# Performance work log

Hardware: AMD Instinct MI355X
Metric: run time of the kernel (lower is better)

## Reference

```python
import jax, jax.numpy as jnp
import numpy as np

INPUT_DIM = 2048
CLASSES = 1000
BATCH = 8192


def setup_inputs() -> dict:
    key = jax.random.key(0)
    kx, ky, kwx, kbx, kwy, kby = jax.random.split(key, 6)
    s_in = 1.0 / np.sqrt(INPUT_DIM)
    return {
        "x": jax.random.normal(kx, (BATCH, INPUT_DIM), dtype=jnp.float32),
        "y": jax.random.normal(ky, (BATCH, INPUT_DIM), dtype=jnp.float32),
        "Wx": jax.random.uniform(kwx, (CLASSES, INPUT_DIM), jnp.float32, -s_in, s_in),
        "bx": jax.random.uniform(kbx, (CLASSES,), jnp.float32, -s_in, s_in),
        "Wy": jax.random.uniform(kwy, (CLASSES, INPUT_DIM), jnp.float32, -s_in, s_in),
        "by": jax.random.uniform(kby, (CLASSES,), jnp.float32, -s_in, s_in),
    }


def _ds_combin_two(alpha1, alpha2, classes):
    # alpha1, alpha2: [B, C] Dirichlet params
    S1 = jnp.sum(alpha1, axis=1, keepdims=True)  # [B,1]
    S2 = jnp.sum(alpha2, axis=1, keepdims=True)
    b1 = (alpha1 - 1.0) / S1                      # belief masses [B,C]
    b2 = (alpha2 - 1.0) / S2
    u1 = classes / S1                             # uncertainty [B,1]
    u2 = classes / S2
    # bb_sum = sum_{i,j} b1_i b2_j = (sum b1)(sum b2); bb_diag = sum_i b1_i b2_i
    bb_sum = jnp.sum(b1, axis=1) * jnp.sum(b2, axis=1)   # [B]
    bb_diag = jnp.sum(b1 * b2, axis=1)                    # [B]
    C = (bb_sum - bb_diag)[:, None]                       # conflict [B,1]
    denom = 1.0 - C
    b_a = (b1 * b2 + b1 * u2 + b2 * u1) / denom           # [B,C]
    u_a = (u1 * u2) / denom                               # [B,1]
    S_a = classes / u_a                                   # [B,1]
    return b_a * S_a + 1.0                                # alpha_a [B,C]


def reference(x, y, Wx, bx, Wy, by):
    out_x = x @ Wx.T + bx                 # [B,C]
    out_y = y @ Wy.T + by
    alpha_x = jax.nn.softplus(out_x) + 1.0
    alpha_y = jax.nn.softplus(out_y) + 1.0
    alpha_a = _ds_combin_two(alpha_x, alpha_y, CLASSES)
    return (alpha_a, alpha_x, alpha_y)
```

## Files before the change

kernel.cpp:

```cpp
#include <hip/hip_runtime.h>
#include <hip/hip_bf16.h>
#include <math.h>

#define BATCH_N 8192
#define K_DIM   2048
#define CLS     1000

typedef __attribute__((ext_vector_type(8))) short short8;
typedef __attribute__((ext_vector_type(8))) unsigned short ushort8;
typedef __attribute__((ext_vector_type(4))) float floatx4;

static __device__ __forceinline__ float softplus_fast(float z) {
    return fmaxf(z, 0.f) + __logf(1.f + __expf(-fabsf(z)));
}


constexpr int NT = K_DIM / 32;

#define BARX  __builtin_amdgcn_s_barrier()
#define LGKM0 asm volatile("s_waitcnt lgkmcnt(0)" ::: "memory")
#define SB0   __builtin_amdgcn_sched_barrier(0)
#define PRIO1 __builtin_amdgcn_s_setprio(1)
#define PRIO0 __builtin_amdgcn_s_setprio(0)

__global__ __launch_bounds__(256, 2)
void gemm_fused(const float* __restrict__ Xa, const float* __restrict__ Xb,
                const float* __restrict__ Wa, const float* __restrict__ Wb,
                const float* __restrict__ biasa, const float* __restrict__ biasb,
                float* __restrict__ outa, float* __restrict__ outb)
{
    int flat = blockIdx.x + 8 * (blockIdx.y + 64 * blockIdx.z);
    int sw   = (flat & 7) * 128 + (flat >> 3);
    const int bx = sw & 7, by = (sw >> 3) & 63, bz = sw >> 9;

    const float* A    = bz ? Xb : Xa;
    const float* B    = bz ? Wb : Wa;
    const float* bias = bz ? biasb : biasa;
    float* out        = bz ? outb : outa;

    __shared__ ushort As[2][128 * 32];
    __shared__ ushort Bs[2][128 * 32];

    const int tid  = threadIdx.x;
    const int lane = tid & 63;
    const int wid  = tid >> 6;
    const int wr = wid >> 1, wc = wid & 1;
    const int fr = lane & 15, fg = lane >> 4;
    const int brow = by * 128;
    const int bcol = bx * 128;

    size_t a_g[2], b_g[2];
    int    l_of[2];
#pragma unroll
    for (int i = 0; i < 2; ++i) {
        int q = tid + i * 256;
        int p = q >> 3, c8 = q & 7, c8l = c8 ^ (p & 7);
        int r = 2 * p + (c8l >> 2);
        int k = (c8l & 3) * 8;
        a_g[i] = (size_t)(brow + r) * K_DIM + k;
        int wrow = bcol + r; if (wrow >= CLS) wrow = CLS - 1;
        b_g[i] = (size_t)wrow * K_DIM + k;
        l_of[i] = q * 8;
    }

    int afoff[4], bfoff[4];
#pragma unroll
    for (int m = 0; m < 4; ++m) {
        int row = wr * 64 + m * 16 + fr;
        int p = row >> 1;
        int c = (((row & 1) << 2) | fg) ^ (p & 7);
        afoff[m] = (p * 8 + c) * 8;
    }
#pragma unroll
    for (int n = 0; n < 4; ++n) {
        int row = wc * 64 + n * 16 + fr;
        int p = row >> 1;
        int c = (((row & 1) << 2) | fg) ^ (p & 7);
        bfoff[n] = (p * 8 + c) * 8;
    }

    floatx4 acc[4][4];
#pragma unroll
    for (int m = 0; m < 4; ++m)
#pragma unroll
        for (int n = 0; n < 4; ++n)
            acc[m][n] = (floatx4){0.f, 0.f, 0.f, 0.f};

    float4 ga[2][2], gb[2][2];

#define LOADT(t_) {                                                           \
    const size_t kb_ = (size_t)(t_) * 32;                                     \
    ga[0][0] = *(const float4*)(A + a_g[0] + kb_);                            \
    ga[0][1] = *(const float4*)(A + a_g[0] + kb_ + 4);                        \
    ga[1][0] = *(const float4*)(A + a_g[1] + kb_);                            \
    ga[1][1] = *(const float4*)(A + a_g[1] + kb_ + 4);                        \
    gb[0][0] = *(const float4*)(B + b_g[0] + kb_);                            \
    gb[0][1] = *(const float4*)(B + b_g[0] + kb_ + 4);                        \
    gb[1][0] = *(const float4*)(B + b_g[1] + kb_);                            \
    gb[1][1] = *(const float4*)(B + b_g[1] + kb_ + 4);                        \
}

#define CVTW(sl_) {                                                           \
    _Pragma("unroll")                                                         \
    for (int i = 0; i < 2; ++i) {                                             \
        ushort8 ta, tb;                                                       \
        _Pragma("unroll")                                                     \
        for (int j = 0; j < 4; ++j) {                                         \
            ta[j]     = __hip_bfloat16_raw(__float2bfloat16(((const float*)&ga[i][0])[j])).x; \
            ta[j + 4] = __hip_bfloat16_raw(__float2bfloat16(((const float*)&ga[i][1])[j])).x; \
            tb[j]     = __hip_bfloat16_raw(__float2bfloat16(((const float*)&gb[i][0])[j])).x; \
            tb[j + 4] = __hip_bfloat16_raw(__float2bfloat16(((const float*)&gb[i][1])[j])).x; \
        }                                                                     \
        *(ushort8*)&As[sl_][l_of[i]] = ta;                                    \
        *(ushort8*)&Bs[sl_][l_of[i]] = tb;                                    \
    }                                                                         \
}

    LOADT(0)
    CVTW(0)
    LOADT(1)
    SB0; LGKM0; BARX; SB0;

#pragma unroll 1
    for (int t = 0; t < NT; ++t) {
        const ushort* asl = &As[t & 1][0];
        const ushort* bsl = &Bs[t & 1][0];
        short8 af[4], bf[4];
#pragma unroll
        for (int m = 0; m < 4; ++m) af[m] = *(const short8*)(asl + afoff[m]);
#pragma unroll
        for (int n = 0; n < 4; ++n) bf[n] = *(const short8*)(bsl + bfoff[n]);

        PRIO1;
#pragma unroll
        for (int m = 0; m < 4; ++m)
#pragma unroll
            for (int n = 0; n < 4; ++n)
                acc[m][n] = __builtin_amdgcn_mfma_f32_16x16x32_bf16(
                    af[m], bf[n], acc[m][n], 0, 0, 0);
        PRIO0;

        if (t + 1 < NT) CVTW((t + 1) & 1)
        if (t + 2 < NT) LOADT(t + 2)
        SB0; LGKM0; BARX; SB0;
    }

#pragma unroll
    for (int n = 0; n < 4; ++n) {
        int col = bcol + wc * 64 + n * 16 + fr;
        if (col >= CLS) continue;
        float bv = bias[col];
#pragma unroll
        for (int m = 0; m < 4; ++m) {
#pragma unroll
            for (int j = 0; j < 4; ++j) {
                int row = brow + wr * 64 + m * 16 + fg * 4 + j;
                float z = acc[m][n][j] + bv;
                out[(size_t)row * CLS + col] = softplus_fast(z) + 1.f;
            }
        }
    }
}


__global__ __launch_bounds__(256)
void ds_combine(const float* __restrict__ AX, const float* __restrict__ AY,
                float* __restrict__ out)
{
    const int row = blockIdx.x * 4 + (threadIdx.x >> 6);
    const int l = threadIdx.x & 63;
    const float* ax = AX + (size_t)row * CLS;
    const float* ay = AY + (size_t)row * CLS;

    float4 vx[4], vy[4];
    float sx = 0.f, sy = 0.f, sp = 0.f;
#pragma unroll
    for (int c = 0; c < 4; ++c) {
        int idx = l + c * 64;
        if (idx < CLS / 4) {
            vx[c] = *(const float4*)(ax + idx * 4);
            vy[c] = *(const float4*)(ay + idx * 4);
            const float* px = (const float*)&vx[c];
            const float* py = (const float*)&vy[c];
#pragma unroll
            for (int j = 0; j < 4; ++j) {
                sx += px[j]; sy += py[j];
                sp += (px[j] - 1.f) * (py[j] - 1.f);
            }
        }
    }
#pragma unroll
    for (int off = 1; off < 64; off <<= 1) {
        sx += __shfl_xor(sx, off);
        sy += __shfl_xor(sy, off);
        sp += __shfl_xor(sp, off);
    }
    const float S1 = sx, S2 = sy, P = sp;
    const float i1 = 1.f / S1, i2 = 1.f / S2;
    const float u1 = (float)CLS * i1, u2 = (float)CLS * i2;
    const float sb1 = (S1 - (float)CLS) * i1;
    const float sb2 = (S2 - (float)CLS) * i2;
    const float conf = sb1 * sb2 - P * i1 * i2;
    const float denom = 1.f - conf;
    const float idenom = 1.f / denom;
    const float Sa = (float)CLS * denom / (u1 * u2);

#pragma unroll
    for (int c = 0; c < 4; ++c) {
        int idx = l + c * 64;
        if (idx < CLS / 4) {
            float4 vo;
            const float* px = (const float*)&vx[c];
            const float* py = (const float*)&vy[c];
            float* po = (float*)&vo;
#pragma unroll
            for (int j = 0; j < 4; ++j) {
                float b1 = (px[j] - 1.f) * i1;
                float b2 = (py[j] - 1.f) * i2;
                float ba = (b1 * b2 + b1 * u2 + b2 * u1) * idenom;
                po[j] = ba * Sa + 1.f;
            }
            *(float4*)(out + (size_t)row * CLS + idx * 4) = vo;
        }
    }
}

extern "C" void kernel_launch(void* const* d_in, const int* in_sizes, int n_in,
                              void* d_out, int out_size, void* d_ws, size_t ws_size,
                              hipStream_t stream) {
    const float* x  = (const float*)d_in[0];
    const float* y  = (const float*)d_in[1];
    const float* Wx = (const float*)d_in[2];
    const float* bx = (const float*)d_in[3];
    const float* Wy = (const float*)d_in[4];
    const float* by = (const float*)d_in[5];
    float* out = (float*)d_out;
    float* ax = out + (size_t)BATCH_N * CLS;
    float* ay = ax  + (size_t)BATCH_N * CLS;

    gemm_fused<<<dim3(8, 64, 2), 256, 0, stream>>>(
        x, y, Wx, Wy, bx, by, ax, ay);
    ds_combine<<<BATCH_N / 4, 256, 0, stream>>>(ax, ay, out);
}
```

Measured before the change: 131.1 us.

## Enlarge GEMM block tile to 256x128 with 512 threads

Doubles the block tile along the batch dimension to 256 rows using 512 threads (8 waves), so each staged B (weight) tile is shared by twice as many rows. Load and convert logic is reorganized so A takes two chunks per thread and B one. This halves the grid, reduces redundant weight reads and conversions per output, and raises LDS use per block. The risk is lower occupancy and fewer blocks (512) across the CUs.

New measurement: 124.6 us. 1.05x faster.

```diff
diff --git a/kernel.cpp b/kernel.cpp
--- a/kernel.cpp
+++ b/kernel.cpp
@@ -14,8 +14,9 @@
     return fmaxf(z, 0.f) + __logf(1.f + __expf(-fabsf(z)));
 }
 
-
-constexpr int NT = K_DIM / 32;
+static __device__ __forceinline__ ushort f2bfr(float f) {
+    return __hip_bfloat16_raw(__float2bfloat16(f)).x;
+}
 
 #define BARX  __builtin_amdgcn_s_barrier()
 #define LGKM0 asm volatile("s_waitcnt lgkmcnt(0)" ::: "memory")
@@ -23,22 +24,25 @@
 #define PRIO1 __builtin_amdgcn_s_setprio(1)
 #define PRIO0 __builtin_amdgcn_s_setprio(0)
 
-__global__ __launch_bounds__(256, 2)
+constexpr int NT = K_DIM / 32;
+
+
+__global__ __launch_bounds__(512, 2)
 void gemm_fused(const float* __restrict__ Xa, const float* __restrict__ Xb,
                 const float* __restrict__ Wa, const float* __restrict__ Wb,
                 const float* __restrict__ biasa, const float* __restrict__ biasb,
                 float* __restrict__ outa, float* __restrict__ outb)
 {
-    int flat = blockIdx.x + 8 * (blockIdx.y + 64 * blockIdx.z);
-    int sw   = (flat & 7) * 128 + (flat >> 3);
-    const int bx = sw & 7, by = (sw >> 3) & 63, bz = sw >> 9;
+    int flat = blockIdx.x + 8 * (blockIdx.y + 32 * blockIdx.z);
+    int sw   = (flat & 7) * 64 + (flat >> 3);
+    const int bx = sw & 7, by = (sw >> 3) & 31, bz = sw >> 8;
 
     const float* A    = bz ? Xb : Xa;
     const float* B    = bz ? Wb : Wa;
     const float* bias = bz ? biasb : biasa;
     float* out        = bz ? outb : outa;
 
-    __shared__ ushort As[2][128 * 32];
+    __shared__ ushort As[2][256 * 32];
     __shared__ ushort Bs[2][128 * 32];
 
     const int tid  = threadIdx.x;
@@ -46,21 +50,26 @@
     const int wid  = tid >> 6;
     const int wr = wid >> 1, wc = wid & 1;
     const int fr = lane & 15, fg = lane >> 4;
-    const int brow = by * 128;
+    const int brow = by * 256;
     const int bcol = bx * 128;
 
-    size_t a_g[2], b_g[2];
-    int    l_of[2];
+    size_t a_g[2], b_g;
+    int    a_l[2], b_l;
 #pragma unroll
     for (int i = 0; i < 2; ++i) {
-        int q = tid + i * 256;
+        int q = tid + i * 512;
         int p = q >> 3, c8 = q & 7, c8l = c8 ^ (p & 7);
         int r = 2 * p + (c8l >> 2);
-        int k = (c8l & 3) * 8;
-        a_g[i] = (size_t)(brow + r) * K_DIM + k;
+        a_g[i] = (size_t)(brow + r) * K_DIM + (c8l & 3) * 8;
+        a_l[i] = q * 8;
+    }
+    {
+        int q = tid;
+        int p = q >> 3, c8 = q & 7, c8l = c8 ^ (p & 7);
+        int r = 2 * p + (c8l >> 2);
         int wrow = bcol + r; if (wrow >= CLS) wrow = CLS - 1;
-        b_g[i] = (size_t)wrow * K_DIM + k;
-        l_of[i] = q * 8;
+        b_g = (size_t)wrow * K_DIM + (c8l & 3) * 8;
+        b_l = q * 8;
     }
 
     int afoff[4], bfoff[4];
@@ -86,7 +95,7 @@
         for (int n = 0; n < 4; ++n)
             acc[m][n] = (floatx4){0.f, 0.f, 0.f, 0.f};
 
-    float4 ga[2][2], gb[2][2];
+    float4 ga[2][2], gb[2];
 
 #define LOADT(t_) {                                                           \
     const size_t kb_ = (size_t)(t_) * 32;                                     \
@@ -94,26 +103,28 @@
     ga[0][1] = *(const float4*)(A + a_g[0] + kb_ + 4);                        \
     ga[1][0] = *(const float4*)(A + a_g[1] + kb_);                            \
     ga[1][1] = *(const float4*)(A + a_g[1] + kb_ + 4);                        \
-    gb[0][0] = *(const float4*)(B + b_g[0] + kb_);                            \
-    gb[0][1] = *(const float4*)(B + b_g[0] + kb_ + 4);                        \
-    gb[1][0] = *(const float4*)(B + b_g[1] + kb_);                            \
-    gb[1][1] = *(const float4*)(B + b_g[1] + kb_ + 4);                        \
+    gb[0]    = *(const float4*)(B + b_g + kb_);                               \
+    gb[1]    = *(const float4*)(B + b_g + kb_ + 4);                           \
 }
 
 #define CVTW(sl_) {                                                           \
     _Pragma("unroll")                                                         \
     for (int i = 0; i < 2; ++i) {                                             \
-        ushort8 ta, tb;                                                       \
+        ushort8 ta;                                                           \
         _Pragma("unroll")                                                     \
         for (int j = 0; j < 4; ++j) {                                         \
-            ta[j]     = __hip_bfloat16_raw(__float2bfloat16(((const float*)&ga[i][0])[j])).x; \
-            ta[j + 4] = __hip_bfloat16_raw(__float2bfloat16(((const float*)&ga[i][1])[j])).x; \
-            tb[j]     = __hip_bfloat16_raw(__float2bfloat16(((const float*)&gb[i][0])[j])).x; \
-            tb[j + 4] = __hip_bfloat16_raw(__float2bfloat16(((const float*)&gb[i][1])[j])).x; \
+            ta[j]     = f2bfr(((const float*)&ga[i][0])[j]);                  \
+            ta[j + 4] = f2bfr(((const float*)&ga[i][1])[j]);                  \
         }                                                                     \
-        *(ushort8*)&As[sl_][l_of[i]] = ta;                                    \
-        *(ushort8*)&Bs[sl_][l_of[i]] = tb;                                    \
+        *(ushort8*)&As[sl_][a_l[i]] = ta;                                     \
     }                                                                         \
+    ushort8 tb;                                                               \
+    _Pragma("unroll")                                                         \
+    for (int j = 0; j < 4; ++j) {                                             \
+        tb[j]     = f2bfr(((const float*)&gb[0])[j]);                         \
+        tb[j + 4] = f2bfr(((const float*)&gb[1])[j]);                         \
+    }                                                                         \
+    *(ushort8*)&Bs[sl_][b_l] = tb;                                            \
 }
 
     LOADT(0)
@@ -238,7 +249,7 @@
     float* ax = out + (size_t)BATCH_N * CLS;
     float* ay = ax  + (size_t)BATCH_N * CLS;
 
-    gemm_fused<<<dim3(8, 64, 2), 256, 0, stream>>>(
+    gemm_fused<<<dim3(8, 32, 2), 512, 0, stream>>>(
         x, y, Wx, Wy, bx, by, ax, ay);
     ds_combine<<<BATCH_N / 4, 256, 0, stream>>>(ax, ay, out);
 }
```
